# Performance work log

Measured on AMD Instinct MI355X. Metric: run time of the kernel, lower is better.

The kernel has to match this reference:

```python
import jax, jax.numpy as jnp
import numpy as np

DIM = 128
EDGE_FEAT_DIM = 2
N_NODES = 50000
N_EDGES = 600000
EPS = 1e-5


def setup_inputs() -> dict:
    key = jax.random.key(0)
    ks = jax.random.split(key, 16)
    d = DIM
    inp = {}
    inp["x"] = jax.random.normal(ks[0], (N_NODES, d), dtype=jnp.float32)
    inp["edge_index"] = jax.random.randint(ks[1], (2, N_EDGES), 0, N_NODES, dtype=jnp.int32)
    inp["edge_weight_norm"] = jax.random.uniform(ks[2], (N_EDGES,), dtype=jnp.float32)
    inp["edge_feat"] = jax.random.normal(ks[3], (N_EDGES, EDGE_FEAT_DIM), dtype=jnp.float32)
    inp["batch"] = jnp.zeros((N_NODES,), dtype=jnp.int32)
    # phi: Linear(dim, dim)
    inp["W_phi"] = jax.random.normal(ks[4], (d, d), dtype=jnp.float32) * (1.0 / np.sqrt(d))
    inp["b_phi"] = jnp.zeros((d,), dtype=jnp.float32)
    # edge_gate: Linear(2d+2, d) -> BN(d) -> GELU -> Linear(d, 1)
    din = 2 * d + EDGE_FEAT_DIM
    inp["W_g1"] = jax.random.normal(ks[5], (din, d), dtype=jnp.float32) * (1.0 / np.sqrt(din))
    inp["b_g1"] = jnp.zeros((d,), dtype=jnp.float32)
    inp["bn_gamma"] = jnp.ones((d,), dtype=jnp.float32)
    inp["bn_beta"] = jnp.zeros((d,), dtype=jnp.float32)
    inp["bn_mean"] = jnp.zeros((d,), dtype=jnp.float32)
    inp["bn_var"] = jnp.ones((d,), dtype=jnp.float32)
    inp["W_g2"] = jax.random.normal(ks[6], (d, 1), dtype=jnp.float32) * (1.0 / np.sqrt(d))
    inp["b_g2"] = jnp.zeros((1,), dtype=jnp.float32)
    # upd: Linear(2d, d)
    inp["W_u"] = jax.random.normal(ks[7], (2 * d, d), dtype=jnp.float32) * (1.0 / np.sqrt(2 * d))
    inp["b_u"] = jnp.zeros((d,), dtype=jnp.float32)
    # LayerNorm(dim)
    inp["ln_gamma"] = jnp.ones((d,), dtype=jnp.float32)
    inp["ln_beta"] = jnp.zeros((d,), dtype=jnp.float32)
    return inp


def reference(x, edge_index, edge_weight_norm, edge_feat, batch,
              W_phi, b_phi, W_g1, b_g1, bn_gamma, bn_beta, bn_mean, bn_var,
              W_g2, b_g2, W_u, b_u, ln_gamma, ln_beta):
    src, dst = edge_index[0], edge_index[1]
    # phi(x): [N, d]
    xj = x @ W_phi + b_phi
    # edge gate MLP on [x_dst, x_src, e]: [E, 2d+2]
    g_in = jnp.concatenate([x[dst], x[src], edge_feat], axis=-1)
    h1 = g_in @ W_g1 + b_g1
    h1 = (h1 - bn_mean) * jax.lax.rsqrt(bn_var + EPS) * bn_gamma + bn_beta  # BN eval mode
    h1 = jax.nn.gelu(h1, approximate=False)
    gate = jax.nn.sigmoid(h1 @ W_g2 + b_g2)[:, 0]  # [E]
    # messages and scatter-add aggregation
    msg = xj[src] * (edge_weight_norm * gate)[:, None]  # [E, d]
    agg = jax.ops.segment_sum(msg, dst, num_segments=x.shape[0])  # [N, d]
    # update MLP + GELU + residual + LayerNorm
    h = jnp.concatenate([x, agg], axis=-1) @ W_u + b_u
    h = jax.nn.gelu(h, approximate=False)
    y = x + h
    mu = jnp.mean(y, axis=-1, keepdims=True)
    var = jnp.var(y, axis=-1, keepdims=True)
    return (y - mu) * jax.lax.rsqrt(var + EPS) * ln_gamma + ln_beta
```

## Files before the change

### kernel.cpp

```cpp
#include <hip/hip_runtime.h>
#include <hip/hip_fp16.h>
#include <math.h>

#define DIM 128
#define NN 50000
#define NE 600000
#define EPS 1e-5f
#define CAP 64
#define NB_NODE 782
#define NB_EDGE 586

struct H8 { __half2 h[4]; };
struct F8 { float4 a, b; };

typedef _Float16 f16x8 __attribute__((ext_vector_type(8)));
typedef float    f32x4 __attribute__((ext_vector_type(4)));

__device__ __forceinline__ float gelu_fast(float x) {
    const float c1 = 2.3022085f;
    const float c2 = 0.1029437f;
    const float x2 = x * x;
    const float z  = x * __builtin_fmaf(c2, x2, c1);
    const float u  = __builtin_amdgcn_exp2f(z);
    const float r  = __builtin_amdgcn_rcpf(1.f + u);
    return __builtin_fmaf(-x, r, x);
}

__device__ __forceinline__ float sigmoid_fast(float y) {
    const float u = __builtin_amdgcn_exp2f(-1.4426950409f * y);
    return __builtin_amdgcn_rcpf(1.f + u);
}

__global__ __launch_bounds__(256) void k_prep_scale(
    const float* __restrict__ Wg1, const float* __restrict__ bg1,
    const float* __restrict__ bng, const float* __restrict__ bnb,
    const float* __restrict__ bnm, const float* __restrict__ bnv,
    __half* __restrict__ WABth, float* __restrict__ bA,
    float* __restrict__ w0p, float* __restrict__ w1p)
{
    const int k = blockIdx.x;
    const int t = threadIdx.x;
    const int c = t & 127;
    const float s = bng[c] * rsqrtf(bnv[c] + EPS);
    const float w = (t < 128) ? Wg1[k * DIM + c] : Wg1[(DIM + k) * DIM + c];
    WABth[t * DIM + k] = __float2half(w * s);
    if (k == 0 && t < 128) {
        const float tt = bnb[c] - bnm[c] * s;
        bA[c]  = bg1[c] * s + tt;
        w0p[c] = Wg1[256 * DIM + c] * s;
        w1p[c] = Wg1[257 * DIM + c] * s;
    }
}

__global__ __launch_bounds__(128) void k_prep_wpu(
    const float* __restrict__ Wphi, const float* __restrict__ bphi,
    const float* __restrict__ Wu,
    __half* __restrict__ Wct, float* __restrict__ bpu)
{
    const int a = blockIdx.x;
    const int j = threadIdx.x;
    float acc = 0.f;
    #pragma unroll 8
    for (int k = 0; k < DIM; ++k)
        acc += Wphi[a * DIM + k] * Wu[(DIM + k) * DIM + j];
    Wct[j * 256 + a]       = __float2half(Wu[a * DIM + j]);
    Wct[j * 256 + 128 + a] = __float2half(acc);
    if (a == 0) {
        float b = 0.f;
        #pragma unroll 8
        for (int k = 0; k < DIM; ++k)
            b += bphi[k] * Wu[(DIM + k) * DIM + j];
        bpu[j] = b;
    }
}

__global__ __launch_bounds__(256) void k_node_bucket(
    const float* __restrict__ x, const __half* __restrict__ WABth,
    const float* __restrict__ bA,
    const int* __restrict__ ei, const float* __restrict__ ew,
    const float* __restrict__ ef,
    __half* __restrict__ A, __half* __restrict__ Bv, __half* __restrict__ xh,
    int* __restrict__ deg, int2* __restrict__ rec)
{
    __shared__ __half tile[64][264];

    if (blockIdx.x >= NB_NODE) {
        const int tid = (blockIdx.x - NB_NODE) * 256 + threadIdx.x;
        #pragma unroll
        for (int k = 0; k < 4; ++k) {
            const int e = tid + k * (NB_EDGE * 256);
            if (e < NE) {
                const int s = ei[e];
                const int d = ei[NE + e];
                const float2 efv = *(const float2*)(ef + 2 * e);
                const int ewq = (int)fminf(ew[e] * 32768.f + 0.5f, 32767.f);
                int2 r;
                r.x = s | (ewq << 17);
                r.y = (int)__half_as_ushort(__float2half(efv.x)) |
                      ((int)__half_as_ushort(__float2half(efv.y)) << 16);
                const int pos = atomicAdd(&deg[d], 1);
                if (pos < CAP)
                    rec[(size_t)d * CAP + pos] = r;
            }
        }
        return;
    }

    const int t    = threadIdx.x;
    const int wv   = t >> 6;
    const int lane = t & 63;
    const int n16  = lane & 15;
    const int quad = lane >> 4;
    const int m0   = blockIdx.x * 64;

    f32x4 acc[4][4];
    #pragma unroll
    for (int mt = 0; mt < 4; ++mt)
        #pragma unroll
        for (int nt = 0; nt < 4; ++nt)
            acc[mt][nt] = (f32x4){0.f, 0.f, 0.f, 0.f};

    int rowm[4];
    #pragma unroll
    for (int mt = 0; mt < 4; ++mt)
        rowm[mt] = min(m0 + mt * 16 + n16, NN - 1);

    #pragma unroll
    for (int ks = 0; ks < 4; ++ks) {
        const int ko = ks * 32 + quad * 8;
        f16x8 bf[4];
        #pragma unroll
        for (int nt = 0; nt < 4; ++nt) {
            const int c = wv * 64 + nt * 16 + n16;
            bf[nt] = *(const f16x8*)(WABth + c * DIM + ko);
        }
        #pragma unroll
        for (int mt = 0; mt < 4; ++mt) {
            const float4 xa = *(const float4*)(x + (size_t)rowm[mt] * DIM + ko);
            const float4 xb = *(const float4*)(x + (size_t)rowm[mt] * DIM + ko + 4);
            f16x8 af;
            af[0] = (_Float16)xa.x; af[1] = (_Float16)xa.y;
            af[2] = (_Float16)xa.z; af[3] = (_Float16)xa.w;
            af[4] = (_Float16)xb.x; af[5] = (_Float16)xb.y;
            af[6] = (_Float16)xb.z; af[7] = (_Float16)xb.w;
            if (wv == 0)
                *(f16x8*)(xh + (size_t)rowm[mt] * DIM + ko) = af;
            #pragma unroll
            for (int nt = 0; nt < 4; ++nt)
                acc[mt][nt] = __builtin_amdgcn_mfma_f32_16x16x32_f16(
                    af, bf[nt], acc[mt][nt], 0, 0, 0);
        }
    }

    #pragma unroll
    for (int nt = 0; nt < 4; ++nt) {
        const int c = wv * 64 + nt * 16 + n16;
        const float bias = (c < 128) ? bA[c] : 0.f;
        #pragma unroll
        for (int mt = 0; mt < 4; ++mt)
            #pragma unroll
            for (int reg = 0; reg < 4; ++reg)
                tile[mt * 16 + quad * 4 + reg][c] =
                    __float2half(acc[mt][nt][reg] + bias);
    }
    __syncthreads();

    #pragma unroll
    for (int i = 0; i < 8; ++i) {
        const int chunk = t + i * 256;
        const int row = chunk >> 5;
        const int o   = (chunk & 31) * 8;
        if (m0 + row < NN) {
            const uint4 v = *(const uint4*)&tile[row][o];
            if (o < 128) *(uint4*)(A  + (size_t)(m0 + row) * DIM + o)       = v;
            else         *(uint4*)(Bv + (size_t)(m0 + row) * DIM + o - 128) = v;
        }
    }
}

__global__ __launch_bounds__(256) void k_gate2(
    const int* __restrict__ deg, int2* __restrict__ rec,
    const __half* __restrict__ A, const __half* __restrict__ Bv,
    const float* __restrict__ w0p, const float* __restrict__ w1p,
    const float* __restrict__ Wg2, const float* __restrict__ bg2)
{
    const int n = blockIdx.x;
    const int d = min(deg[n], CAP);
    const int t    = threadIdx.x;
    const int wv   = t >> 6;
    if (16 * wv >= d) return;

    const int lane = t & 63;
    const int sub  = lane >> 4;
    const int sl   = lane & 15;
    const int c8   = sl * 8;
    const int e0   = (4 * wv + sub) * 4;

    const H8 ar = *(const H8*)(A + (size_t)n * DIM + c8);

    const F8 W0 = *(const F8*)(w0p + c8);
    const F8 W1 = *(const F8*)(w1p + c8);
    const F8 WG = *(const F8*)(Wg2 + c8);
    const float bg2v = bg2[0];
    const float* w0 = (const float*)&W0;
    const float* w1 = (const float*)&W1;
    const float* wg = (const float*)&WG;

    const size_t base = (size_t)n * CAP;

    #pragma unroll
    for (int s = 0; s < 2; ++s) {
        const int j0 = e0 + 2 * s;
        if (j0 >= d) break;
        const bool v1 = (j0 + 1 < d);

        const int4 pq = *(const int4*)(&rec[base + j0]);
        const int sx0 = pq.x & 0x1FFFF;
        const int sx1 = v1 ? (pq.z & 0x1FFFF) : 0;
        const float ew0 = (float)((unsigned)pq.x >> 17) * (1.f / 32768.f);
        const float ew1 = v1 ? (float)((unsigned)pq.z >> 17) * (1.f / 32768.f) : 0.f;
        const float2 ef0 = __half22float2(*(const __half2*)&pq.y);
        const float2 ef1 = __half22float2(*(const __half2*)&pq.w);

        const H8 b0 = *(const H8*)(Bv + (size_t)sx0 * DIM + c8);
        const H8 b1 = *(const H8*)(Bv + (size_t)sx1 * DIM + c8);

        float p0 = 0.f, p1 = 0.f;
        #pragma unroll
        for (int i = 0; i < 4; ++i) {
            const float2 s0 = __half22float2(__hadd2(ar.h[i], b0.h[i]));
            const float2 s1 = __half22float2(__hadd2(ar.h[i], b1.h[i]));
            const int c0 = 2 * i, c1 = 2 * i + 1;
            float h;
            h = s0.x + ef0.x * w0[c0] + ef0.y * w1[c0];
            p0 = __builtin_fmaf(gelu_fast(h), wg[c0], p0);
            h = s0.y + ef0.x * w0[c1] + ef0.y * w1[c1];
            p0 = __builtin_fmaf(gelu_fast(h), wg[c1], p0);
            h = s1.x + ef1.x * w0[c0] + ef1.y * w1[c0];
            p1 = __builtin_fmaf(gelu_fast(h), wg[c0], p1);
            h = s1.y + ef1.x * w0[c1] + ef1.y * w1[c1];
            p1 = __builtin_fmaf(gelu_fast(h), wg[c1], p1);
        }
        #pragma unroll
        for (int off = 1; off < 16; off <<= 1) {
            p0 += __shfl_xor(p0, off, 64);
            p1 += __shfl_xor(p1, off, 64);
        }

        if (sl == 0) {
            rec[base + j0].y = __float_as_int(ew0 * sigmoid_fast(p0 + bg2v));
            if (v1)
                rec[base + j0 + 1].y = __float_as_int(ew1 * sigmoid_fast(p1 + bg2v));
        }
    }
}

__global__ __launch_bounds__(128, 3) void k_agg_update(
    const int* __restrict__ deg, const int2* __restrict__ rec,
    const __half* __restrict__ xh, const __half* __restrict__ Wct,
    const float* __restrict__ bu, const float* __restrict__ bpu,
    const float* __restrict__ lng, const float* __restrict__ lnb,
    float* __restrict__ out)
{
    __shared__ __half xt[16][136];
    __shared__ __half at[2][16][136];
    __shared__ float  sct[2][16];
    __shared__ float  sred_s[2][16];
    __shared__ float  sred_ss[2][16];

    const int t    = threadIdx.x;
    const int w    = t >> 6;
    const int lane = t & 63;
    const int n16  = lane & 15;
    const int quad = lane >> 4;
    const int m0   = blockIdx.x * 16;

    const int slot = quad;
    const int sl   = n16;
    const int c8   = sl * 8;

    int    cnt[4];
    size_t pb[4];
    #pragma unroll
    for (int r = 0; r < 4; ++r) {
        const int lr = r * 4 + slot;
        const int nc = min(m0 + lr, NN - 1);
        const int d  = min(deg[nc], CAP);
        const int h  = ((d + 2) >> 2) << 1;
        const int lo = w ? h : 0;
        const int hi = w ? d : h;
        cnt[r] = hi - lo;
        pb[r]  = (size_t)nc * CAP + lo;
    }

    #pragma unroll
    for (int i = 0; i < 2; ++i) {
        const int idx = i * 128 + t;
        const int row = idx >> 4;
        const int col = (idx & 15) * 8;
        const int grow = min(m0 + row, NN - 1);
        *(f16x8*)&xt[row][col] = *(const f16x8*)(xh + (size_t)grow * DIM + col);
    }

    float acc[4][8];
    float scn[4] = {0.f, 0.f, 0.f, 0.f};
    #pragma unroll
    for (int r = 0; r < 4; ++r)
        #pragma unroll
        for (int i = 0; i < 8; ++i) acc[r][i] = 0.f;

    const int cmax = max(max(cnt[0], cnt[1]), max(cnt[2], cnt[3]));

    for (int jj = 0; jj < cmax; jj += 4) {
        int4 pq0[4], pq1[4];
        #pragma unroll
        for (int r = 0; r < 4; ++r) {
            pq0[r] = *(const int4*)(&rec[pb[r] + jj]);
            pq1[r] = *(const int4*)(&rec[pb[r] + jj + 2]);
        }

        int   ix[16];
        float cf[16];
        #pragma unroll
        for (int r = 0; r < 4; ++r) {
            const int q = 4 * r;
            const bool v0 = (jj     < cnt[r]);
            const bool v1 = (jj + 1 < cnt[r]);
            const bool v2 = (jj + 2 < cnt[r]);
            const bool v3 = (jj + 3 < cnt[r]);
            ix[q]     = v0 ? (pq0[r].x & 0x1FFFF) : 0;
            cf[q]     = v0 ? __int_as_float(pq0[r].y) : 0.f;
            ix[q + 1] = v1 ? (pq0[r].z & 0x1FFFF) : 0;
            cf[q + 1] = v1 ? __int_as_float(pq0[r].w) : 0.f;
            ix[q + 2] = v2 ? (pq1[r].x & 0x1FFFF) : 0;
            cf[q + 2] = v2 ? __int_as_float(pq1[r].y) : 0.f;
            ix[q + 3] = v3 ? (pq1[r].z & 0x1FFFF) : 0;
            cf[q + 3] = v3 ? __int_as_float(pq1[r].w) : 0.f;
        }

        H8 xv[16];
        #pragma unroll
        for (int q = 0; q < 16; ++q)
            xv[q] = *(const H8*)(xh + (size_t)ix[q] * DIM + c8);

        #pragma unroll
        for (int r = 0; r < 4; ++r) {
            #pragma unroll
            for (int k = 0; k < 4; ++k) {
                const int   q = 4 * r + k;
                const float c = cf[q];
                #pragma unroll
                for (int i = 0; i < 4; ++i) {
                    const float2 f = __half22float2(xv[q].h[i]);
                    acc[r][2 * i]     = __builtin_fmaf(c, f.x, acc[r][2 * i]);
                    acc[r][2 * i + 1] = __builtin_fmaf(c, f.y, acc[r][2 * i + 1]);
                }
                scn[r] += c;
            }
        }
    }

    #pragma unroll
    for (int r = 0; r < 4; ++r) {
        const int lr = r * 4 + slot;
        f16x8 hv;
        #pragma unroll
        for (int i = 0; i < 8; ++i) hv[i] = (_Float16)acc[r][i];
        *(f16x8*)&at[w][lr][c8] = hv;
        if (sl == 0) sct[w][lr] = scn[r];
    }
    __syncthreads();

    f32x4 acc2[4];
    #pragma unroll
    for (int nt = 0; nt < 4; ++nt) acc2[nt] = (f32x4){0.f, 0.f, 0.f, 0.f};

    const int rloc = n16;
    #pragma unroll
    for (int ks = 0; ks < 4; ++ks) {
        const int ko = ks * 32 + quad * 8;
        const f16x8 af = *(const f16x8*)&xt[rloc][ko];
        #pragma unroll
        for (int nt = 0; nt < 4; ++nt) {
            const int c = w * 64 + nt * 16 + n16;
            const f16x8 bf = *(const f16x8*)(Wct + c * 256 + ko);
            acc2[nt] = __builtin_amdgcn_mfma_f32_16x16x32_f16(af, bf, acc2[nt], 0, 0, 0);
        }
    }
    #pragma unroll
    for (int half = 0; half < 2; ++half) {
        #pragma unroll
        for (int ks = 0; ks < 4; ++ks) {
            const int ko = ks * 32 + quad * 8;
            const f16x8 af = *(const f16x8*)&at[half][rloc][ko];
            #pragma unroll
            for (int nt = 0; nt < 4; ++nt) {
                const int c = w * 64 + nt * 16 + n16;
                const f16x8 bf = *(const f16x8*)(Wct + c * 256 + 128 + ko);
                acc2[nt] = __builtin_amdgcn_mfma_f32_16x16x32_f16(af, bf, acc2[nt], 0, 0, 0);
            }
        }
    }

    int   rl[4];
    float scv[4];
    #pragma unroll
    for (int reg = 0; reg < 4; ++reg) {
        rl[reg]  = quad * 4 + reg;
        scv[reg] = sct[0][rl[reg]] + sct[1][rl[reg]];
    }

    float yv[4][4];
    float s[4]  = {0.f, 0.f, 0.f, 0.f};
    float ss[4] = {0.f, 0.f, 0.f, 0.f};

    #pragma unroll
    for (int nt = 0; nt < 4; ++nt) {
        const int c = w * 64 + nt * 16 + n16;
        const float buv = bu[c], bpv = bpu[c];
        #pragma unroll
        for (int reg = 0; reg < 4; ++reg) {
            float h = acc2[nt][reg] + buv + scv[reg] * bpv;
            h = gelu_fast(h);
            const float xv = __half2float(xt[rl[reg]][c]);
            const float y = xv + h;
            yv[nt][reg] = y;
            s[reg]  += y;
            ss[reg] += y * y;
        }
    }

    #pragma unroll
    for (int reg = 0; reg < 4; ++reg) {
        #pragma unroll
        for (int off = 1; off < 16; off <<= 1) {
            s[reg]  += __shfl_xor(s[reg],  off, 64);
            ss[reg] += __shfl_xor(ss[reg], off, 64);
        }
    }
    if (n16 == 0) {
        #pragma unroll
        for (int reg = 0; reg < 4; ++reg) {
            sred_s[w][rl[reg]]  = s[reg];
            sred_ss[w][rl[reg]] = ss[reg];
        }
    }
    __syncthreads();

    float mu[4], rs[4];
    #pragma unroll
    for (int reg = 0; reg < 4; ++reg) {
        const float stot  = sred_s[0][rl[reg]]  + sred_s[1][rl[reg]];
        const float sstot = sred_ss[0][rl[reg]] + sred_ss[1][rl[reg]];
        mu[reg] = stot * (1.f / DIM);
        const float var = sstot * (1.f / DIM) - mu[reg] * mu[reg];
        rs[reg] = rsqrtf(var + EPS);
    }

    #pragma unroll
    for (int nt = 0; nt < 4; ++nt) {
        const int c = w * 64 + nt * 16 + n16;
        const float gg = lng[c], bb2 = lnb[c];
        #pragma unroll
        for (int reg = 0; reg < 4; ++reg) {
            const int grow = m0 + rl[reg];
            if (grow < NN)
                __builtin_nontemporal_store(
                    (yv[nt][reg] - mu[reg]) * rs[reg] * gg + bb2,
                    &out[(size_t)grow * DIM + c]);
        }
    }
}

extern "C" void kernel_launch(void* const* d_in, const int* in_sizes, int n_in,
                              void* d_out, int out_size, void* d_ws, size_t ws_size,
                              hipStream_t stream)
{
    const float* x    = (const float*)d_in[0];
    const int*   ei   = (const int*)  d_in[1];
    const float* ew   = (const float*)d_in[2];
    const float* ef   = (const float*)d_in[3];
    const float* Wphi = (const float*)d_in[5];
    const float* bphi = (const float*)d_in[6];
    const float* Wg1  = (const float*)d_in[7];
    const float* bg1  = (const float*)d_in[8];
    const float* bng  = (const float*)d_in[9];
    const float* bnb  = (const float*)d_in[10];
    const float* bnm  = (const float*)d_in[11];
    const float* bnv  = (const float*)d_in[12];
    const float* Wg2  = (const float*)d_in[13];
    const float* bg2  = (const float*)d_in[14];
    const float* Wu   = (const float*)d_in[15];
    const float* bu   = (const float*)d_in[16];
    const float* lng  = (const float*)d_in[17];
    const float* lnb  = (const float*)d_in[18];

    float* out = (float*)d_out;

    char* wsb = (char*)d_ws;
    size_t off = 0;
    auto carve = [&](size_t bytes) -> void* {
        void* p = wsb + off;
        off += (bytes + 255) & ~(size_t)255;
        return p;
    };
    __half* xh    = (__half*)carve((size_t)NN * DIM * 2);
    __half* A     = (__half*)carve((size_t)NN * DIM * 2);
    __half* Bv    = (__half*)carve((size_t)NN * DIM * 2);
    __half* WABth = (__half*)carve(256 * DIM * 2);
    __half* Wct   = (__half*)carve(DIM * 256 * 2);
    float*  bA    = (float*) carve(DIM * 4);
    float*  w0p   = (float*) carve(DIM * 4);
    float*  w1p   = (float*) carve(DIM * 4);
    float*  bpu   = (float*) carve(DIM * 4);
    int*    deg   = (int*)   carve((size_t)NN * 4);
    int2*   rec   = (int2*)  carve((size_t)NN * CAP * 8 + 256);

    hipMemsetAsync(deg, 0, (size_t)NN * 4, stream);

    k_prep_scale<<<128, 256, 0, stream>>>(Wg1, bg1, bng, bnb, bnm, bnv,
                                          WABth, bA, w0p, w1p);
    k_prep_wpu<<<128, 128, 0, stream>>>(Wphi, bphi, Wu, Wct, bpu);
    k_node_bucket<<<NB_NODE + NB_EDGE, 256, 0, stream>>>(
        x, WABth, bA, ei, ew, ef, A, Bv, xh, deg, rec);
    k_gate2<<<NN, 256, 0, stream>>>(deg, rec, A, Bv, w0p, w1p, Wg2, bg2);
    k_agg_update<<<(NN + 15) / 16, 128, 0, stream>>>(deg, rec, xh, Wct,
                                                     bu, bpu, lng, lnb, out);
}
```

Measured before the change: 293.0 us.

## Merge prep kernels with edge bucketing, stage x in LDS, one wave per node in gate

```diff
diff --git a/kernel.cpp b/kernel.cpp
--- a/kernel.cpp
+++ b/kernel.cpp
@@ -7,7 +7,7 @@
 #define NE 600000
 #define EPS 1e-5f
 #define CAP 64
-#define NB_NODE 782
+#define NB_PREP 256
 #define NB_EDGE 586
 
 struct H8 { __half2 h[4]; };
@@ -31,61 +31,52 @@
     return __builtin_amdgcn_rcpf(1.f + u);
 }
 
-__global__ __launch_bounds__(256) void k_prep_scale(
+__global__ __launch_bounds__(256) void k_prep_bucket(
     const float* __restrict__ Wg1, const float* __restrict__ bg1,
     const float* __restrict__ bng, const float* __restrict__ bnb,
     const float* __restrict__ bnm, const float* __restrict__ bnv,
-    __half* __restrict__ WABth, float* __restrict__ bA,
-    float* __restrict__ w0p, float* __restrict__ w1p)
-{
-    const int k = blockIdx.x;
-    const int t = threadIdx.x;
-    const int c = t & 127;
-    const float s = bng[c] * rsqrtf(bnv[c] + EPS);
-    const float w = (t < 128) ? Wg1[k * DIM + c] : Wg1[(DIM + k) * DIM + c];
-    WABth[t * DIM + k] = __float2half(w * s);
-    if (k == 0 && t < 128) {
-        const float tt = bnb[c] - bnm[c] * s;
-        bA[c]  = bg1[c] * s + tt;
-        w0p[c] = Wg1[256 * DIM + c] * s;
-        w1p[c] = Wg1[257 * DIM + c] * s;
-    }
-}
-
-__global__ __launch_bounds__(128) void k_prep_wpu(
     const float* __restrict__ Wphi, const float* __restrict__ bphi,
     const float* __restrict__ Wu,
-    __half* __restrict__ Wct, float* __restrict__ bpu)
-{
-    const int a = blockIdx.x;
-    const int j = threadIdx.x;
-    float acc = 0.f;
-    #pragma unroll 8
-    for (int k = 0; k < DIM; ++k)
-        acc += Wphi[a * DIM + k] * Wu[(DIM + k) * DIM + j];
-    Wct[j * 256 + a]       = __float2half(Wu[a * DIM + j]);
-    Wct[j * 256 + 128 + a] = __float2half(acc);
-    if (a == 0) {
-        float b = 0.f;
-        #pragma unroll 8
-        for (int k = 0; k < DIM; ++k)
-            b += bphi[k] * Wu[(DIM + k) * DIM + j];
-        bpu[j] = b;
-    }
-}
-
-__global__ __launch_bounds__(256) void k_node_bucket(
-    const float* __restrict__ x, const __half* __restrict__ WABth,
-    const float* __restrict__ bA,
     const int* __restrict__ ei, const float* __restrict__ ew,
     const float* __restrict__ ef,
-    __half* __restrict__ A, __half* __restrict__ Bv, __half* __restrict__ xh,
+    __half* __restrict__ WABth, float* __restrict__ bA,
+    float* __restrict__ w0p, float* __restrict__ w1p,
+    __half* __restrict__ Wct, float* __restrict__ bpu,
     int* __restrict__ deg, int2* __restrict__ rec)
 {
-    __shared__ __half tile[64][264];
-
-    if (blockIdx.x >= NB_NODE) {
-        const int tid = (blockIdx.x - NB_NODE) * 256 + threadIdx.x;
+    if (blockIdx.x < 128) {
+        const int k = blockIdx.x;
+        const int t = threadIdx.x;
+        const int c = t & 127;
+        const float s = bng[c] * rsqrtf(bnv[c] + EPS);
+        const float w = (t < 128) ? Wg1[k * DIM + c] : Wg1[(DIM + k) * DIM + c];
+        WABth[t * DIM + k] = __float2half(w * s);
+        if (k == 0 && t < 128) {
+            const float tt = bnb[c] - bnm[c] * s;
+            bA[c]  = bg1[c] * s + tt;
+            w0p[c] = Wg1[256 * DIM + c] * s;
+            w1p[c] = Wg1[257 * DIM + c] * s;
+        }
+    } else if (blockIdx.x < NB_PREP) {
+        const int a = blockIdx.x - 128;
+        const int j = threadIdx.x;
+        if (j < 128) {
+            float acc = 0.f;
+            #pragma unroll 8
+            for (int k = 0; k < DIM; ++k)
+                acc += Wphi[a * DIM + k] * Wu[(DIM + k) * DIM + j];
+            Wct[j * 256 + a]       = __float2half(Wu[a * DIM + j]);
+            Wct[j * 256 + 128 + a] = __float2half(acc);
+            if (a == 0) {
+                float b = 0.f;
+                #pragma unroll 8
+                for (int k = 0; k < DIM; ++k)
+                    b += bphi[k] * Wu[(DIM + k) * DIM + j];
+                bpu[j] = b;
+            }
+        }
+    } else {
+        const int tid = (blockIdx.x - NB_PREP) * 256 + threadIdx.x;
         #pragma unroll
         for (int k = 0; k < 4; ++k) {
             const int e = tid + k * (NB_EDGE * 256);
@@ -103,8 +94,16 @@
                     rec[(size_t)d * CAP + pos] = r;
             }
         }
-        return;
-    }
+    }
+}
+
+__global__ __launch_bounds__(256) void k_node_mfma(
+    const float* __restrict__ x, const __half* __restrict__ WABth,
+    const float* __restrict__ bA,
+    __half* __restrict__ A, __half* __restrict__ Bv, __half* __restrict__ xh)
+{
+    __shared__ __half xs[64][136];
+    __shared__ __half ys[64][136];
 
     const int t    = threadIdx.x;
     const int wv   = t >> 6;
@@ -113,17 +112,30 @@
     const int quad = lane >> 4;
     const int m0   = blockIdx.x * 64;
 
+    #pragma unroll
+    for (int i = 0; i < 4; ++i) {
+        const int idx = i * 256 + t;
+        const int row = idx >> 4;
+        const int col = (idx & 15) * 8;
+        const int grow = min(m0 + row, NN - 1);
+        const float4 xa = *(const float4*)(x + (size_t)grow * DIM + col);
+        const float4 xb = *(const float4*)(x + (size_t)grow * DIM + col + 4);
+        f16x8 af;
+        af[0] = (_Float16)xa.x; af[1] = (_Float16)xa.y;
+        af[2] = (_Float16)xa.z; af[3] = (_Float16)xa.w;
+        af[4] = (_Float16)xb.x; af[5] = (_Float16)xb.y;
+        af[6] = (_Float16)xb.z; af[7] = (_Float16)xb.w;
+        *(f16x8*)&xs[row][col] = af;
+        *(f16x8*)(xh + (size_t)grow * DIM + col) = af;
+    }
+    __syncthreads();
+
     f32x4 acc[4][4];
     #pragma unroll
     for (int mt = 0; mt < 4; ++mt)
         #pragma unroll
         for (int nt = 0; nt < 4; ++nt)
             acc[mt][nt] = (f32x4){0.f, 0.f, 0.f, 0.f};
-
-    int rowm[4];
-    #pragma unroll
-    for (int mt = 0; mt < 4; ++mt)
-        rowm[mt] = min(m0 + mt * 16 + n16, NN - 1);
 
     #pragma unroll
     for (int ks = 0; ks < 4; ++ks) {
@@ -136,21 +148,14 @@
         }
         #pragma unroll
         for (int mt = 0; mt < 4; ++mt) {
-            const float4 xa = *(const float4*)(x + (size_t)rowm[mt] * DIM + ko);
-            const float4 xb = *(const float4*)(x + (size_t)rowm[mt] * DIM + ko + 4);
-            f16x8 af;
-            af[0] = (_Float16)xa.x; af[1] = (_Float16)xa.y;
-            af[2] = (_Float16)xa.z; af[3] = (_Float16)xa.w;
-            af[4] = (_Float16)xb.x; af[5] = (_Float16)xb.y;
-            af[6] = (_Float16)xb.z; af[7] = (_Float16)xb.w;
-            if (wv == 0)
-                *(f16x8*)(xh + (size_t)rowm[mt] * DIM + ko) = af;
+            const f16x8 af = *(const f16x8*)&xs[mt * 16 + n16][ko];
             #pragma unroll
             for (int nt = 0; nt < 4; ++nt)
                 acc[mt][nt] = __builtin_amdgcn_mfma_f32_16x16x32_f16(
                     af, bf[nt], acc[mt][nt], 0, 0, 0);
         }
     }
+    __syncthreads();
 
     #pragma unroll
     for (int nt = 0; nt < 4; ++nt) {
@@ -159,9 +164,12 @@
         #pragma unroll
         for (int mt = 0; mt < 4; ++mt)
             #pragma unroll
-            for (int reg = 0; reg < 4; ++reg)
-                tile[mt * 16 + quad * 4 + reg][c] =
-                    __float2half(acc[mt][nt][reg] + bias);
+            for (int reg = 0; reg < 4; ++reg) {
+                const int row = mt * 16 + quad * 4 + reg;
+                const __half hv = __float2half(acc[mt][nt][reg] + bias);
+                if (c < 128) xs[row][c]       = hv;
+                else         ys[row][c - 128] = hv;
+            }
     }
     __syncthreads();
 
@@ -171,9 +179,13 @@
         const int row = chunk >> 5;
         const int o   = (chunk & 31) * 8;
         if (m0 + row < NN) {
-            const uint4 v = *(const uint4*)&tile[row][o];
-            if (o < 128) *(uint4*)(A  + (size_t)(m0 + row) * DIM + o)       = v;
-            else         *(uint4*)(Bv + (size_t)(m0 + row) * DIM + o - 128) = v;
+            if (o < 128) {
+                const uint4 v = *(const uint4*)&xs[row][o];
+                *(uint4*)(A + (size_t)(m0 + row) * DIM + o) = v;
+            } else {
+                const uint4 v = *(const uint4*)&ys[row][o - 128];
+                *(uint4*)(Bv + (size_t)(m0 + row) * DIM + o - 128) = v;
+            }
         }
     }
 }
@@ -184,17 +196,16 @@
     const float* __restrict__ w0p, const float* __restrict__ w1p,
     const float* __restrict__ Wg2, const float* __restrict__ bg2)
 {
-    const int n = blockIdx.x;
-    const int d = min(deg[n], CAP);
-    const int t    = threadIdx.x;
-    const int wv   = t >> 6;
-    if (16 * wv >= d) return;
+    const int t  = threadIdx.x;
+    const int wv = t >> 6;
+    const int n  = blockIdx.x * 4 + wv;
+    const int d  = min(deg[n], CAP);
+    if (d == 0) return;
 
     const int lane = t & 63;
     const int sub  = lane >> 4;
     const int sl   = lane & 15;
     const int c8   = sl * 8;
-    const int e0   = (4 * wv + sub) * 4;
 
     const H8 ar = *(const H8*)(A + (size_t)n * DIM + c8);
 
@@ -208,10 +219,7 @@
 
     const size_t base = (size_t)n * CAP;
 
-    #pragma unroll
-    for (int s = 0; s < 2; ++s) {
-        const int j0 = e0 + 2 * s;
-        if (j0 >= d) break;
+    for (int j0 = sub * 2; j0 < d; j0 += 8) {
         const bool v1 = (j0 + 1 < d);
 
         const int4 pq = *(const int4*)(&rec[base + j0]);
@@ -518,12 +526,11 @@
 
     hipMemsetAsync(deg, 0, (size_t)NN * 4, stream);
 
-    k_prep_scale<<<128, 256, 0, stream>>>(Wg1, bg1, bng, bnb, bnm, bnv,
-                                          WABth, bA, w0p, w1p);
-    k_prep_wpu<<<128, 128, 0, stream>>>(Wphi, bphi, Wu, Wct, bpu);
-    k_node_bucket<<<NB_NODE + NB_EDGE, 256, 0, stream>>>(
-        x, WABth, bA, ei, ew, ef, A, Bv, xh, deg, rec);
-    k_gate2<<<NN, 256, 0, stream>>>(deg, rec, A, Bv, w0p, w1p, Wg2, bg2);
+    k_prep_bucket<<<NB_PREP + NB_EDGE, 256, 0, stream>>>(
+        Wg1, bg1, bng, bnb, bnm, bnv, Wphi, bphi, Wu, ei, ew, ef,
+        WABth, bA, w0p, w1p, Wct, bpu, deg, rec);
+    k_node_mfma<<<(NN + 63) / 64, 256, 0, stream>>>(x, WABth, bA, A, Bv, xh);
+    k_gate2<<<NN / 4, 256, 0, stream>>>(deg, rec, A, Bv, w0p, w1p, Wg2, bg2);
     k_agg_update<<<(NN + 15) / 16, 128, 0, stream>>>(deg, rec, xh, Wct,
                                                      bu, bpu, lng, lnb, out);
 }
```

Measured after the change: 268.8 us. 1.09x faster.
